# Optimization experiments

Measured on AMD Instinct MI355X. Metric: run time of the kernel, lower is better.

Reference implementation:

```python
import jax, jax.numpy as jnp
import numpy as np

B, C_IN, C_OUT = 16, 256, 128
V_RAW, N_VERT, K = 10242, 40962, 7


def setup_inputs() -> dict:
    key = jax.random.key(0)
    k1, k2, k3, k4, k5, k6 = jax.random.split(key, 6)
    x = jax.random.normal(k1, (B, C_IN, V_RAW), dtype=jnp.float32)
    W = jax.random.normal(k2, (C_OUT, C_IN), dtype=jnp.float32) * (1.0 / np.sqrt(C_IN))
    b = jax.random.normal(k3, (C_OUT,), dtype=jnp.float32) * 0.01
    up_neigh_indices = jax.random.randint(k4, (N_VERT, K), 0, N_VERT, dtype=jnp.int64)
    down_indices = jax.random.randint(k5, (V_RAW,), 0, N_VERT, dtype=jnp.int64)
    max_pool_indices = jax.random.randint(k6, (B, C_OUT, V_RAW), 0, K, dtype=jnp.int64)
    return {"x": x, "W": W, "b": b,
            "up_neigh_indices": up_neigh_indices,
            "down_indices": down_indices,
            "max_pool_indices": max_pool_indices}


def _feats_indices(n_feats: int, n_raw_vertices: int) -> np.ndarray:
    # torch: floor(linspace(0, n_feats, num=n_raw_vertices*n_feats)); last -= 1
    fi = np.floor(np.linspace(0.0, float(n_feats), num=n_raw_vertices * n_feats))
    fi[-1] -= 1
    return fi.astype(np.int64)


def reference(x, W, b, up_neigh_indices, down_indices, max_pool_indices):
    n_samples, in_feats, n_raw = x.shape
    n_vertices = up_neigh_indices.shape[0]
    out_feats = W.shape[0]

    # per-vertex linear projection: (B, Cin, V) -> (B, Cout, V)
    h = jnp.einsum('bcv,oc->bov', x, W) + b[None, :, None]

    # neighbor table at coarse vertices: (V_raw, K)
    neigh = up_neigh_indices[down_indices]

    # vertices_indices[b, f, v] = neigh[v, max_pool_indices[b, f, v]]
    vi = neigh[jnp.arange(n_raw)[None, None, :], max_pool_indices]  # (B, Cout, V_raw)

    # flatten exactly like torch (row-major over (Cout, V_raw))
    h_flat = h.reshape(n_samples, out_feats * n_raw)
    vi_flat = vi.reshape(n_samples, out_feats * n_raw)
    fi = jnp.asarray(_feats_indices(out_feats, n_raw))  # (Cout*V_raw,) static

    y = jnp.zeros((n_samples, out_feats, n_vertices), dtype=h.dtype)
    y = y.at[jnp.arange(n_samples)[:, None], fi[None, :], vi_flat].set(h_flat)
    return y
```

## Files before the change

kernel.cpp:

```cpp
#include <hip/hip_runtime.h>

#define NB    16
#define CIN   256
#define COUT  128
#define VRAW  10242
#define NVERT 40962
#define HALF  20481

typedef __attribute__((ext_vector_type(8))) short short8;
typedef __attribute__((ext_vector_type(4))) float floatx4;

__device__ inline unsigned short f2bf(float f) {
    unsigned u = __builtin_bit_cast(unsigned, f);
    u += 0x7fffu + ((u >> 16) & 1u);
    return (unsigned short)(u >> 16);
}

__global__ __launch_bounds__(256) void convw_kernel(const float* __restrict__ W,
                                                    unsigned short* __restrict__ Wbf) {
    int i = blockIdx.x * 256 + threadIdx.x;
    Wbf[i] = f2bf(W[i]);
}

__global__ __launch_bounds__(256) void gemm_kernel(const float* __restrict__ x,
                                                   const unsigned short* __restrict__ Wbf,
                                                   const float* __restrict__ bias,
                                                   float* __restrict__ h) {
    const int b    = blockIdx.y;
    const int v0   = blockIdx.x * 128;
    const int wave = threadIdx.x >> 6;
    const int lane = threadIdx.x & 63;
    const int mn   = lane & 15;
    const int q    = lane >> 4;

    const int vw = v0 + wave * 32;

    floatx4 acc[8][2];
#pragma unroll
    for (int ot = 0; ot < 8; ot++) { acc[ot][0] = (floatx4)0.f; acc[ot][1] = (floatx4)0.f; }

#pragma unroll
    for (int ck = 0; ck < 8; ck++) {
        const int c0 = ck * 32;
        short8 bfrag[2];
#pragma unroll
        for (int vt = 0; vt < 2; vt++) {
            const int v   = vw + vt * 16 + mn;
            const bool ok = v < VRAW;
            const float* xp = x + ((size_t)b * CIN + (c0 + q * 8)) * VRAW + v;
#pragma unroll
            for (int j = 0; j < 8; j++) {
                float xv = ok ? xp[(size_t)j * VRAW] : 0.f;
                bfrag[vt][j] = (short)f2bf(xv);
            }
        }
#pragma unroll
        for (int ot = 0; ot < 8; ot++) {
            short8 afrag = *(const short8*)(Wbf + (ot * 16 + mn) * CIN + c0 + q * 8);
            acc[ot][0] = __builtin_amdgcn_mfma_f32_16x16x32_bf16(afrag, bfrag[0], acc[ot][0], 0, 0, 0);
            acc[ot][1] = __builtin_amdgcn_mfma_f32_16x16x32_bf16(afrag, bfrag[1], acc[ot][1], 0, 0, 0);
        }
    }

#pragma unroll
    for (int ot = 0; ot < 8; ot++) {
#pragma unroll
        for (int vt = 0; vt < 2; vt++) {
            const int v = vw + vt * 16 + mn;
            if (v < VRAW) {
#pragma unroll
                for (int r = 0; r < 4; r++) {
                    const int o = ot * 16 + q * 4 + r;
                    h[((size_t)b * COUT + o) * VRAW + v] = acc[ot][vt][r] + bias[o];
                }
            }
        }
    }
}

__global__ __launch_bounds__(1024) void scatter_kernel(const int* __restrict__ up,
                                                       const int* __restrict__ down,
                                                       const int* __restrict__ mpi,
                                                       const float* __restrict__ h,
                                                       float* __restrict__ y) {
    __shared__ unsigned st[(HALF + 1) / 2];
    const int r     = blockIdx.x >> 1;
    const int tbase = (blockIdx.x & 1) * HALF;
    const int tid   = threadIdx.x;

    for (int i = tid; i < (HALF + 1) / 2; i += 1024) st[i] = 0u;
    __syncthreads();

    const int* mpiRow = mpi + (size_t)r * VRAW;
    for (int v = tid; v < VRAW; v += 1024) {
        const int k = mpiRow[v];
        const int t = up[down[v] * 7 + k];
        const unsigned lt = (unsigned)(t - tbase);
        if (lt < (unsigned)HALF) {
            const unsigned val = (unsigned)(v + 1);
            const unsigned sh  = (lt & 1u) * 16u;
            unsigned* p = &st[lt >> 1];
            unsigned old = *p;
            while (true) {
                unsigned cur = (old >> sh) & 0xffffu;
                if (cur >= val) break;
                unsigned nw = (old & ~(0xffffu << sh)) | (val << sh);
                unsigned prev = atomicCAS(p, old, nw);
                if (prev == old) break;
                old = prev;
            }
        }
    }
    __syncthreads();

    const float* hRow = h + (size_t)r * VRAW;
    float* yRow = y + (size_t)r * NVERT + tbase;
    for (int lt = tid; lt < HALF; lt += 1024) {
        const unsigned s = (st[(unsigned)lt >> 1] >> (((unsigned)lt & 1u) * 16u)) & 0xffffu;
        yRow[lt] = s ? hRow[s - 1] : 0.0f;
    }
}

extern "C" void kernel_launch(void* const* d_in, const int* in_sizes, int n_in,
                              void* d_out, int out_size, void* d_ws, size_t ws_size,
                              hipStream_t stream) {
    const float* x    = (const float*)d_in[0];
    const float* W    = (const float*)d_in[1];
    const float* bias = (const float*)d_in[2];
    const int*   up   = (const int*)d_in[3];
    const int*   down = (const int*)d_in[4];
    const int*   mpi  = (const int*)d_in[5];
    float* y = (float*)d_out;

    unsigned short* Wbf = (unsigned short*)d_ws;
    float* h = (float*)((char*)d_ws + 65536);

    convw_kernel<<<COUT * CIN / 256, 256, 0, stream>>>(W, Wbf);

    dim3 ggrid((VRAW + 127) / 128, NB);
    gemm_kernel<<<ggrid, 256, 0, stream>>>(x, Wbf, bias, h);

    scatter_kernel<<<NB * COUT * 2, 1024, 0, stream>>>(up, down, mpi, h, y);
}
```

Measured before the change: 816.0 us.

## Tile GEMM through LDS and restructure scatter with precomputed neighbor table

The GEMM now stages a bf16-converted, swizzled x tile in LDS with vectorized loads and gives each wave a 64x64 output block, which improves reuse over the per-lane strided global loads. A prep kernel precomputes a packed 16-bit neighbor table, so the scatter does one vector load per vertex instead of a dependent double gather. The scatter uses four quarter-blocks with full 32-bit atomicMax in place of a 16-bit CAS loop, plus vectorized LDS reads and output stores. It also remaps block order across rows. The cost is an extra launch, more workspace, and more scatter blocks that each rescan the mpi row.

```diff
diff --git a/kernel.cpp b/kernel.cpp
--- a/kernel.cpp
+++ b/kernel.cpp
@@ -5,10 +5,11 @@
 #define COUT  128
 #define VRAW  10242
 #define NVERT 40962
-#define HALF  20481
+#define QSZ   10241
 
 typedef __attribute__((ext_vector_type(8))) short short8;
 typedef __attribute__((ext_vector_type(4))) float floatx4;
+typedef float f4u __attribute__((ext_vector_type(4), aligned(4)));
 
 __device__ inline unsigned short f2bf(float f) {
     unsigned u = __builtin_bit_cast(unsigned, f);
@@ -22,102 +23,192 @@
     Wbf[i] = f2bf(W[i]);
 }
 
+__global__ __launch_bounds__(256) void prep_kernel(const int* __restrict__ up,
+                                                   const int* __restrict__ down,
+                                                   unsigned short* __restrict__ T16) {
+    int idx = blockIdx.x * 256 + threadIdx.x;
+    if (idx >= VRAW * 8) return;
+    int v = idx >> 3;
+    int k = idx & 7;
+    if (k > 6) k = 6;
+    T16[idx] = (unsigned short)up[down[v] * 7 + k];
+}
+
+#define KC 64
+#define VT 128
 __global__ __launch_bounds__(256) void gemm_kernel(const float* __restrict__ x,
                                                    const unsigned short* __restrict__ Wbf,
                                                    const float* __restrict__ bias,
                                                    float* __restrict__ h) {
+    __shared__ unsigned short xt[VT * KC];
     const int b    = blockIdx.y;
-    const int v0   = blockIdx.x * 128;
-    const int wave = threadIdx.x >> 6;
-    const int lane = threadIdx.x & 63;
+    const int v0   = blockIdx.x * VT;
+    const int tid  = threadIdx.x;
+    const int wv   = tid >> 6;
+    const int lane = tid & 63;
     const int mn   = lane & 15;
     const int q    = lane >> 4;
-
-    const int vw = v0 + wave * 32;
-
-    floatx4 acc[8][2];
-#pragma unroll
-    for (int ot = 0; ot < 8; ot++) { acc[ot][0] = (floatx4)0.f; acc[ot][1] = (floatx4)0.f; }
-
-#pragma unroll
-    for (int ck = 0; ck < 8; ck++) {
-        const int c0 = ck * 32;
-        short8 bfrag[2];
-#pragma unroll
-        for (int vt = 0; vt < 2; vt++) {
-            const int v   = vw + vt * 16 + mn;
-            const bool ok = v < VRAW;
-            const float* xp = x + ((size_t)b * CIN + (c0 + q * 8)) * VRAW + v;
-#pragma unroll
-            for (int j = 0; j < 8; j++) {
-                float xv = ok ? xp[(size_t)j * VRAW] : 0.f;
-                bfrag[vt][j] = (short)f2bf(xv);
-            }
-        }
-#pragma unroll
-        for (int ot = 0; ot < 8; ot++) {
-            short8 afrag = *(const short8*)(Wbf + (ot * 16 + mn) * CIN + c0 + q * 8);
-            acc[ot][0] = __builtin_amdgcn_mfma_f32_16x16x32_bf16(afrag, bfrag[0], acc[ot][0], 0, 0, 0);
-            acc[ot][1] = __builtin_amdgcn_mfma_f32_16x16x32_bf16(afrag, bfrag[1], acc[ot][1], 0, 0, 0);
-        }
-    }
-
-#pragma unroll
-    for (int ot = 0; ot < 8; ot++) {
-#pragma unroll
-        for (int vt = 0; vt < 2; vt++) {
-            const int v = vw + vt * 16 + mn;
-            if (v < VRAW) {
-#pragma unroll
-                for (int r = 0; r < 4; r++) {
-                    const int o = ot * 16 + q * 4 + r;
-                    h[((size_t)b * COUT + o) * VRAW + v] = acc[ot][vt][r] + bias[o];
+    const int ow   = (wv & 1) * 64;
+    const int vwl  = (wv >> 1) * 64;
+
+    floatx4 acc[4][4];
+#pragma unroll
+    for (int ot = 0; ot < 4; ot++)
+#pragma unroll
+        for (int vt = 0; vt < 4; vt++) acc[ot][vt] = (floatx4)0.f;
+
+    for (int c0 = 0; c0 < CIN; c0 += KC) {
+#pragma unroll
+        for (int i = 0; i < 2; i++) {
+            const int tile  = tid + i * 256;
+            const int cg    = tile >> 5;
+            const int vg    = tile & 31;
+            const int vglob = v0 + vg * 4;
+            const float* xp = x + ((size_t)b * CIN + c0 + cg * 4) * VRAW + vglob;
+            float vals[4][4];
+            if (vglob + 3 < VRAW) {
+#pragma unroll
+                for (int cc = 0; cc < 4; cc++) {
+                    f4u rv = *(const f4u*)(xp + (size_t)cc * VRAW);
+                    vals[cc][0] = rv.x; vals[cc][1] = rv.y;
+                    vals[cc][2] = rv.z; vals[cc][3] = rv.w;
                 }
-            }
-        }
-    }
-}
-
-__global__ __launch_bounds__(1024) void scatter_kernel(const int* __restrict__ up,
-                                                       const int* __restrict__ down,
-                                                       const int* __restrict__ mpi,
-                                                       const float* __restrict__ h,
-                                                       float* __restrict__ y) {
-    __shared__ unsigned st[(HALF + 1) / 2];
-    const int r     = blockIdx.x >> 1;
-    const int tbase = (blockIdx.x & 1) * HALF;
+            } else {
+#pragma unroll
+                for (int cc = 0; cc < 4; cc++)
+#pragma unroll
+                    for (int jj = 0; jj < 4; jj++)
+                        vals[cc][jj] = (vglob + jj < VRAW) ? xp[(size_t)cc * VRAW + jj] : 0.f;
+            }
+            const int swbase = (cg ^ ((vg & 7) << 1)) << 2;
+#pragma unroll
+            for (int jj = 0; jj < 4; jj++) {
+                const int vloc = vg * 4 + jj;
+                unsigned long long pk =
+                      (unsigned long long)f2bf(vals[0][jj])
+                    | ((unsigned long long)f2bf(vals[1][jj]) << 16)
+                    | ((unsigned long long)f2bf(vals[2][jj]) << 32)
+                    | ((unsigned long long)f2bf(vals[3][jj]) << 48);
+                *(unsigned long long*)&xt[vloc * KC + swbase] = pk;
+            }
+        }
+        __syncthreads();
+
+#pragma unroll
+        for (int kk = 0; kk < 2; kk++) {
+            short8 bfrag[4];
+#pragma unroll
+            for (int vt = 0; vt < 4; vt++) {
+                const int vloc = vwl + vt * 16 + mn;
+                const int cqb  = kk * 8 + q * 2;
+                const int cq   = cqb ^ (((vloc >> 2) & 7) << 1);
+                bfrag[vt] = *(const short8*)&xt[vloc * KC + (cq << 2)];
+            }
+#pragma unroll
+            for (int ot = 0; ot < 4; ot++) {
+                const short8 afrag = *(const short8*)(Wbf + (size_t)(ow + ot * 16 + mn) * CIN
+                                                      + c0 + kk * 32 + q * 8);
+#pragma unroll
+                for (int vt = 0; vt < 4; vt++)
+                    acc[ot][vt] = __builtin_amdgcn_mfma_f32_16x16x32_bf16(afrag, bfrag[vt], acc[ot][vt], 0, 0, 0);
+            }
+        }
+        __syncthreads();
+    }
+
+#pragma unroll
+    for (int ot = 0; ot < 4; ot++) {
+#pragma unroll
+        for (int r = 0; r < 4; r++) {
+            const int o  = ow + ot * 16 + q * 4 + r;
+            const float bi = bias[o];
+#pragma unroll
+            for (int vt = 0; vt < 4; vt++) {
+                const int v = v0 + vwl + vt * 16 + mn;
+                if (v < VRAW) h[((size_t)b * COUT + o) * VRAW + v] = acc[ot][vt][r] + bi;
+            }
+        }
+    }
+}
+
+__global__ __launch_bounds__(1024, 8) void scatter_kernel(const unsigned short* __restrict__ T16,
+                                                          const int* __restrict__ mpi,
+                                                          const float* __restrict__ h,
+                                                          float* __restrict__ y) {
+    __shared__ __align__(16) unsigned st[QSZ];
+    const int bid = blockIdx.x;
+    const int x8  = bid & 7;
+    const int j   = bid >> 3;
+    const int r   = x8 * 256 + (j >> 2);
+    const int qi  = j & 3;
+    const int tbase = qi * QSZ;
+    const int qlen  = min(QSZ, NVERT - tbase);
     const int tid   = threadIdx.x;
 
-    for (int i = tid; i < (HALF + 1) / 2; i += 1024) st[i] = 0u;
+    uint4* st4 = (uint4*)st;
+    const uint4 z4 = make_uint4(0u, 0u, 0u, 0u);
+    st4[tid] = z4;
+    st4[tid + 1024] = z4;
+    if (tid < 512) st4[tid + 2048] = z4;
+    if (tid == 0) st[10240] = 0u;
     __syncthreads();
 
     const int* mpiRow = mpi + (size_t)r * VRAW;
-    for (int v = tid; v < VRAW; v += 1024) {
+#pragma unroll 2
+    for (int it = 0; it < 10; it++) {
+        const int v = tid + it * 1024;
         const int k = mpiRow[v];
-        const int t = up[down[v] * 7 + k];
-        const unsigned lt = (unsigned)(t - tbase);
-        if (lt < (unsigned)HALF) {
-            const unsigned val = (unsigned)(v + 1);
-            const unsigned sh  = (lt & 1u) * 16u;
-            unsigned* p = &st[lt >> 1];
-            unsigned old = *p;
-            while (true) {
-                unsigned cur = (old >> sh) & 0xffffu;
-                if (cur >= val) break;
-                unsigned nw = (old & ~(0xffffu << sh)) | (val << sh);
-                unsigned prev = atomicCAS(p, old, nw);
-                if (prev == old) break;
-                old = prev;
-            }
-        }
+        const uint4 tt = *(const uint4*)(T16 + (size_t)v * 8);
+        const unsigned w0 = (k & 2) ? tt.y : tt.x;
+        const unsigned w1 = (k & 2) ? tt.w : tt.z;
+        const unsigned wsel = (k & 4) ? w1 : w0;
+        const unsigned t = (wsel >> ((k & 1) * 16)) & 0xffffu;
+        const unsigned lt = t - (unsigned)tbase;
+        if (lt < (unsigned)qlen) atomicMax(&st[lt], (unsigned)(v + 1));
+    }
+    if (tid < 2) {
+        const int v = 10240 + tid;
+        const int k = mpiRow[v];
+        const uint4 tt = *(const uint4*)(T16 + (size_t)v * 8);
+        const unsigned w0 = (k & 2) ? tt.y : tt.x;
+        const unsigned w1 = (k & 2) ? tt.w : tt.z;
+        const unsigned wsel = (k & 4) ? w1 : w0;
+        const unsigned t = (wsel >> ((k & 1) * 16)) & 0xffffu;
+        const unsigned lt = t - (unsigned)tbase;
+        if (lt < (unsigned)qlen) atomicMax(&st[lt], (unsigned)(v + 1));
     }
     __syncthreads();
 
     const float* hRow = h + (size_t)r * VRAW;
     float* yRow = y + (size_t)r * NVERT + tbase;
-    for (int lt = tid; lt < HALF; lt += 1024) {
-        const unsigned s = (st[(unsigned)lt >> 1] >> (((unsigned)lt & 1u) * 16u)) & 0xffffu;
-        yRow[lt] = s ? hRow[s - 1] : 0.0f;
+#pragma unroll
+    for (int i2 = 0; i2 < 2; i2++) {
+        const int i = tid + i2 * 1024;
+        const uint4 s4 = st4[i];
+        f4u out;
+        out.x = s4.x ? hRow[s4.x - 1u] : 0.f;
+        out.y = s4.y ? hRow[s4.y - 1u] : 0.f;
+        out.z = s4.z ? hRow[s4.z - 1u] : 0.f;
+        out.w = s4.w ? hRow[s4.w - 1u] : 0.f;
+        *(f4u*)(yRow + 4 * i) = out;
+    }
+    {
+        const int i = tid + 2048;
+        if (4 * i + 3 < qlen) {
+            const uint4 s4 = st4[i];
+            f4u out;
+            out.x = s4.x ? hRow[s4.x - 1u] : 0.f;
+            out.y = s4.y ? hRow[s4.y - 1u] : 0.f;
+            out.z = s4.z ? hRow[s4.z - 1u] : 0.f;
+            out.w = s4.w ? hRow[s4.w - 1u] : 0.f;
+            *(f4u*)(yRow + 4 * i) = out;
+        }
+    }
+    const int base = qlen & ~3;
+    if (tid < qlen - base) {
+        const int lt = base + tid;
+        const unsigned s = st[lt];
+        yRow[lt] = s ? hRow[s - 1u] : 0.f;
     }
 }
 
@@ -134,11 +225,13 @@
 
     unsigned short* Wbf = (unsigned short*)d_ws;
     float* h = (float*)((char*)d_ws + 65536);
+    unsigned short* T16 = (unsigned short*)((char*)d_ws + 65536 + (size_t)NB * COUT * VRAW * 4);
 
     convw_kernel<<<COUT * CIN / 256, 256, 0, stream>>>(W, Wbf);
-
-    dim3 ggrid((VRAW + 127) / 128, NB);
+    prep_kernel<<<(VRAW * 8 + 255) / 256, 256, 0, stream>>>(up, down, T16);
+
+    dim3 ggrid((VRAW + VT - 1) / VT, NB);
     gemm_kernel<<<ggrid, 256, 0, stream>>>(x, Wbf, bias, h);
 
-    scatter_kernel<<<NB * COUT * 2, 1024, 0, stream>>>(up, down, mpi, h, y);
-}
+    scatter_kernel<<<NB * COUT * 4, 1024, 0, stream>>>(T16, mpi, h, y);
+}
```

After: 697.4 us. 14.5% less time.
